# Performance work log

Hardware: AMD Instinct MI355X
Metric: run time of the kernel (lower is better)

The kernel has to match this reference:

```python
import jax, jax.numpy as jnp
import numpy as np

B, C, H, W = 2, 256, 32, 32
PK, CK = 256, 256


def setup_inputs() -> dict:
    key = jax.random.key(0)
    ks = jax.random.split(key, 9)
    s = 1.0 / np.sqrt(C)
    return {
        'x': jax.random.normal(ks[0], (B, C, H, W), jnp.float32),
        'primary_indices': jax.random.randint(ks[1], (B, PK), 0, B * H * W),
        'compare_indices': jax.random.randint(ks[2], (B, CK), 0, B * H * W),
        'pre_w': jax.random.uniform(ks[3], (3, C, C), jnp.float32, -s, s),
        'pre_b': jax.random.uniform(ks[4], (3, C), jnp.float32, -s, s),
        'post_w': jax.random.uniform(ks[5], (2, C, C), jnp.float32, -s, s),
        'post_b': jax.random.uniform(ks[6], (2, C), jnp.float32, -s, s),
        'post_out_w': jax.random.uniform(ks[7], (2, C), jnp.float32, -s, s),
        'post_out_b': jax.random.uniform(ks[8], (2,), jnp.float32, -s, s),
    }


def reference(x, primary_indices, compare_indices, pre_w, pre_b,
              post_w, post_b, post_out_w, post_out_b):
    # pre_compare: stack of 1x1 convs (c->c->c->c), ReLU between layers
    h = x
    for i in range(3):
        h = jnp.einsum('bchw,oc->bohw', h, pre_w[i]) + pre_b[i][None, :, None, None]
        if i < 2:
            h = jax.nn.relu(h)
    bs, c, hh, ww = h.shape
    # flatten to [bs*h*w, c] node features (matches torch transpose+reshape)
    flat = h.reshape(bs, c, hh * ww).transpose(0, 2, 1).reshape(bs * hh * ww, c)
    # gather primary / compare node features with global flat indices
    xp = flat[primary_indices.reshape(-1)].reshape(bs, -1, c).transpose(0, 2, 1)  # [b,c,pk]
    xc = flat[compare_indices.reshape(-1)].reshape(bs, -1, c).transpose(0, 2, 1)  # [b,c,ck]
    # broadcast pairwise squared difference -> [b,c,pk,ck]
    xx = (xp[:, :, :, None] - xc[:, :, None, :]) ** 2
    # post_compare: 1x1 conv stack c->c->c->2, ReLU between layers
    g = xx
    for i in range(2):
        g = jax.nn.relu(jnp.einsum('bcpq,oc->bopq', g, post_w[i]) + post_b[i][None, :, None, None])
    out = jnp.einsum('bcpq,oc->bopq', g, post_out_w) + post_out_b[None, :, None, None]
    return out  # [b, 2, pk, ck]
```

## Files before the change

kernel.cpp:

```cpp
#include <hip/hip_runtime.h>

typedef unsigned short u16;
typedef short bf16x8 __attribute__((ext_vector_type(8)));
typedef float f32x4 __attribute__((ext_vector_type(4)));
typedef u16 u16x4 __attribute__((ext_vector_type(4)));

__device__ __forceinline__ float b2f(u16 h) {
  unsigned u = ((unsigned)h) << 16;
  return __builtin_bit_cast(float, u);
}
__device__ __forceinline__ u16 f2b(float f) {
  return __builtin_bit_cast(u16, (__bf16)f);
}
__device__ __forceinline__ void gld_lds16(const void* g, void* l) {
  __builtin_amdgcn_global_load_lds(
      (__attribute__((address_space(1))) void*)(g),
      (__attribute__((address_space(3))) void*)(l), 16, 0, 0);
}

__global__ void dense_edge_prep(const float* __restrict__ x,
                                const float* __restrict__ pre_w,
                                const float* __restrict__ post_w,
                                u16* __restrict__ wb, u16* __restrict__ xt) {
  const int blk = blockIdx.x;
  const int t = threadIdx.x;
  if (blk < 160) {
    const int id = blk * 256 + t;
    const int layer = id >> 13;
    const int sid = id & 8191;
    const int m = sid >> 5;
    const int s8 = sid & 31;
    const float* src = (layer < 2) ? (post_w + layer * 65536)
                                   : (pre_w + (layer - 2) * 65536);
    u16* dst = wb + layer * 65536;
    f32x4 a = *(const f32x4*)(src + m * 256 + s8 * 8);
    f32x4 c = *(const f32x4*)(src + m * 256 + s8 * 8 + 4);
    bf16x8 o;
#pragma unroll
    for (int j = 0; j < 4; j++) o[j] = (short)f2b(a[j]);
#pragma unroll
    for (int j = 0; j < 4; j++) o[4 + j] = (short)f2b(c[j]);
    *(bf16x8*)(dst + (s8 * 256 + m) * 8) = o;
  } else {
    __shared__ float tile[32 * 65];
    const int xb = blk - 160;
    const int b = xb >> 7;
    const int ct = (xb >> 4) & 7;
    const int ht = xb & 15;
    const int c0 = ct * 32, hw0 = ht * 64;
#pragma unroll
    for (int rep = 0; rep < 8; rep++) {
      const int idx = rep * 256 + t;
      const int cl = idx >> 6, hl = idx & 63;
      tile[cl * 65 + hl] = x[(b * 256 + c0 + cl) * 1024 + hw0 + hl];
    }
    __syncthreads();
    const int hl = t >> 2, c8 = t & 3;
    bf16x8 o;
#pragma unroll
    for (int i = 0; i < 8; i++) o[i] = (short)f2b(tile[(c8 * 8 + i) * 65 + hl]);
    *(bf16x8*)(xt + (b * 1024 + hw0 + hl) * 256 + c0 + c8 * 8) = o;
  }
}

__global__ __launch_bounds__(256, 2) void dense_edge_pre(
    const u16* __restrict__ xt, const u16* __restrict__ wpre,
    const float* __restrict__ preb, u16* __restrict__ flat) {
  __shared__ u16 feat[2][4096];
  const int t = threadIdx.x;
  const int wv = t >> 6, ln = t & 63;
  const int nb = blockIdx.x * 16;
  const int q4 = ln >> 4, r15 = ln & 15;

#pragma unroll
  for (int i = 0; i < 2; i++) {
    const int slot = wv * 128 + i * 64 + ln;
    const int s8 = slot >> 4, nl = slot & 15;
    gld_lds16(xt + (nb + nl) * 256 + s8 * 8, &feat[0][slot * 8]);
  }
  __syncthreads();

#pragma unroll
  for (int l = 0; l < 3; l++) {
    const u16* wl = wpre + l * 65536;
    f32x4 acc[4];
    f32x4 zero = {0.f, 0.f, 0.f, 0.f};
#pragma unroll
    for (int mt = 0; mt < 4; mt++) acc[mt] = zero;
#pragma unroll
    for (int s = 0; s < 8; s++) {
      bf16x8 bv = *(const bf16x8*)(&feat[l & 1][((s * 4 + q4) * 16 + r15) * 8]);
#pragma unroll
      for (int mt = 0; mt < 4; mt++) {
        bf16x8 av = *(const bf16x8*)(wl + ((s * 4 + q4) * 256 + wv * 64 + mt * 16 + r15) * 8);
        acc[mt] = __builtin_amdgcn_mfma_f32_16x16x32_bf16(av, bv, acc[mt], 0, 0, 0);
      }
    }
    if (l < 2) {
#pragma unroll
      for (int mt = 0; mt < 4; mt++) {
        const int o = wv * 64 + mt * 16 + q4 * 4;
        f32x4 bb = *(const f32x4*)(preb + l * 256 + o);
        u16x4 pk;
#pragma unroll
        for (int r = 0; r < 4; r++) {
          float v = fmaxf(acc[mt][r] + bb[r], 0.f);
          pk[r] = f2b(v);
        }
        *(u16x4*)(&feat[(l + 1) & 1][((o >> 3) * 16 + r15) * 8 + (o & 7)]) = pk;
      }
      __syncthreads();
    } else {
#pragma unroll
      for (int mt = 0; mt < 4; mt++) {
        const int o = wv * 64 + mt * 16 + q4 * 4;
        f32x4 bb = *(const f32x4*)(preb + 512 + o);
        u16x4 pk;
#pragma unroll
        for (int r = 0; r < 4; r++) pk[r] = f2b(acc[mt][r] + bb[r]);
        *(u16x4*)(flat + (nb + r15) * 256 + o) = pk;
      }
    }
  }
}

#define NT 8
__global__ __launch_bounds__(1024, 4) void dense_edge_main(
    const u16* __restrict__ flat, const int* __restrict__ pidx,
    const int* __restrict__ cidx, const u16* __restrict__ w1s,
    const u16* __restrict__ w2s, const float* __restrict__ b1,
    const float* __restrict__ b2, const float* __restrict__ w3,
    const float* __restrict__ b3, float* __restrict__ out) {
  __shared__ u16 xxbuf[16384];
  __shared__ u16 t1buf[16384];
  __shared__ u16 pstage[2048];
  __shared__ u16 qstage[2][2048];
  __shared__ float pbuf[8][2][64];

  const int t = threadIdx.x;
  const int wv = t >> 6;
  const int ln = t & 63;
  const int q4 = ln >> 4, r15 = ln & 15;
  const bool prod = wv < 8;
  const int w8 = wv & 7;
  const int blk = blockIdx.x;
  const int tile0 = blk * NT;
  const int b = tile0 >> 10;
  const int pt = (tile0 >> 5) & 31;
  const int qt0 = tile0 & 31;
  const int p0 = pt * 8;

  const u16* wsrc = prod ? w1s : w2s;
  bf16x8 af_w[2][8];
#pragma unroll
  for (int s = 0; s < 8; s++)
#pragma unroll
    for (int mt = 0; mt < 2; mt++)
      af_w[mt][s] = *(const bf16x8*)(wsrc + ((s * 4 + q4) * 256 + w8 * 32 + mt * 16 + r15) * 8);

  if (prod) {
    const int slot = (w8 & 3) * 64 + ln;
    const int row = slot & 7, cc = slot >> 3;
    if (w8 < 4) {
      const int pn = pidx[b * 256 + p0 + row];
      gld_lds16(flat + pn * 256 + cc * 8, &pstage[slot * 8]);
    } else {
      const int qn = cidx[b * 256 + qt0 * 8 + row];
      gld_lds16(flat + qn * 256 + cc * 8, &qstage[0][slot * 8]);
    }
  }
  __syncthreads();

#pragma unroll 1
  for (int j = 0; j <= NT; j++) {
    if (prod) {
      if (j < NT) {
        const bool restage = (j < NT - 1) && (w8 >= 4);
        int qn_next = 0, rslot = 0;
        if (restage) {
          rslot = (w8 - 4) * 64 + ln;
          qn_next = cidx[b * 256 + (qt0 + j + 1) * 8 + (rslot & 7)];
        }
        const u16* qs = qstage[j & 1];
        const int prow = ln >> 3, qrow = ln & 7;
#pragma unroll
        for (int i = 0; i < 4; i++) {
          const int cc = w8 * 4 + i;
          bf16x8 av = *(const bf16x8*)(&pstage[(cc * 8 + prow) * 8]);
          bf16x8 bv = *(const bf16x8*)(&qs[(cc * 8 + qrow) * 8]);
          bf16x8 ov;
#pragma unroll
          for (int jj = 0; jj < 8; jj++) {
            float d = b2f((u16)av[jj]) - b2f((u16)bv[jj]);
            ov[jj] = (short)f2b(d * d);
          }
          *(bf16x8*)(xxbuf + ((cc)*64 + ln) * 8) = ov;
        }
        if (restage)
          gld_lds16(flat + qn_next * 256 + (rslot >> 3) * 8,
                    &qstage[(j + 1) & 1][rslot * 8]);
      }
    } else if (j > 0) {
      f32x4 acc[2][4];
      {
        f32x4 zero = {0.f, 0.f, 0.f, 0.f};
#pragma unroll
        for (int mt = 0; mt < 2; mt++)
#pragma unroll
          for (int nt = 0; nt < 4; nt++) acc[mt][nt] = zero;
      }
#pragma unroll
      for (int s = 0; s < 8; s++) {
        bf16x8 bfr[4];
#pragma unroll
        for (int nt = 0; nt < 4; nt++)
          bfr[nt] = *(const bf16x8*)(t1buf + ((s * 4 + q4) * 64 + nt * 16 + r15) * 8);
#pragma unroll
        for (int mt = 0; mt < 2; mt++)
#pragma unroll
          for (int nt = 0; nt < 4; nt++)
            acc[mt][nt] = __builtin_amdgcn_mfma_f32_16x16x32_bf16(af_w[mt][s], bfr[nt], acc[mt][nt], 0, 0, 0);
      }
      float part[2][4] = {{0.f, 0.f, 0.f, 0.f}, {0.f, 0.f, 0.f, 0.f}};
#pragma unroll
      for (int mt = 0; mt < 2; mt++) {
        const int o = w8 * 32 + mt * 16 + q4 * 4;
        f32x4 bb = *(const f32x4*)(b2 + o);
        f32x4 w3a = *(const f32x4*)(w3 + o);
        f32x4 w3b = *(const f32x4*)(w3 + 256 + o);
#pragma unroll
        for (int nt = 0; nt < 4; nt++) {
#pragma unroll
          for (int r = 0; r < 4; r++) {
            float v = fmaxf(acc[mt][nt][r] + bb[r], 0.f);
            part[0][nt] += v * w3a[r];
            part[1][nt] += v * w3b[r];
          }
        }
      }
#pragma unroll
      for (int o3 = 0; o3 < 2; o3++)
#pragma unroll
        for (int nt = 0; nt < 4; nt++) {
          part[o3][nt] += __shfl_xor(part[o3][nt], 16, 64);
          part[o3][nt] += __shfl_xor(part[o3][nt], 32, 64);
        }
      if (q4 == 0) {
#pragma unroll
        for (int o3 = 0; o3 < 2; o3++)
#pragma unroll
          for (int nt = 0; nt < 4; nt++)
            pbuf[w8][o3][nt * 16 + r15] = part[o3][nt];
      }
    }
    __syncthreads();

    if (prod) {
      if (j < NT) {
        f32x4 acc[2][4];
        {
          f32x4 zero = {0.f, 0.f, 0.f, 0.f};
#pragma unroll
          for (int mt = 0; mt < 2; mt++)
#pragma unroll
            for (int nt = 0; nt < 4; nt++) acc[mt][nt] = zero;
        }
#pragma unroll
        for (int s = 0; s < 8; s++) {
          bf16x8 bfr[4];
#pragma unroll
          for (int nt = 0; nt < 4; nt++)
            bfr[nt] = *(const bf16x8*)(xxbuf + ((s * 4 + q4) * 64 + nt * 16 + r15) * 8);
#pragma unroll
          for (int mt = 0; mt < 2; mt++)
#pragma unroll
            for (int nt = 0; nt < 4; nt++)
              acc[mt][nt] = __builtin_amdgcn_mfma_f32_16x16x32_bf16(af_w[mt][s], bfr[nt], acc[mt][nt], 0, 0, 0);
        }
#pragma unroll
        for (int mt = 0; mt < 2; mt++) {
          const int o = w8 * 32 + mt * 16 + q4 * 4;
          f32x4 bb = *(const f32x4*)(b1 + o);
#pragma unroll
          for (int nt = 0; nt < 4; nt++) {
            const int nn = nt * 16 + r15;
            u16x4 pk;
#pragma unroll
            for (int r = 0; r < 4; r++) {
              float v = fmaxf(acc[mt][nt][r] + bb[r], 0.f);
              pk[r] = f2b(v);
            }
            *(u16x4*)(t1buf + ((o >> 3) * 64 + nn) * 8 + (o & 7)) = pk;
          }
        }
      }
    } else if (j > 0) {
      if (wv < 10) {
        const int idx = (wv - 8) * 64 + ln;
        const int o3 = idx >> 6;
        const int n = idx & 63;
        float v = b3[o3];
#pragma unroll
        for (int k = 0; k < 8; k++) v += pbuf[k][o3][n];
        out[((b * 2 + o3) * 256 + p0 + (n >> 3)) * 256 + (qt0 + j - 1) * 8 + (n & 7)] = v;
      }
    }
    __syncthreads();
  }
}

extern "C" void kernel_launch(void* const* d_in, const int* in_sizes, int n_in,
                              void* d_out, int out_size, void* d_ws, size_t ws_size,
                              hipStream_t stream) {
  (void)in_sizes; (void)n_in; (void)out_size; (void)ws_size;
  const float* x          = (const float*)d_in[0];
  const int*   pidx       = (const int*)d_in[1];
  const int*   cidx       = (const int*)d_in[2];
  const float* pre_w      = (const float*)d_in[3];
  const float* pre_b      = (const float*)d_in[4];
  const float* post_w     = (const float*)d_in[5];
  const float* post_b     = (const float*)d_in[6];
  const float* post_out_w = (const float*)d_in[7];
  const float* post_out_b = (const float*)d_in[8];
  float* out = (float*)d_out;

  u16* ws   = (u16*)d_ws;
  u16* wb   = ws;
  u16* w1s  = wb;
  u16* w2s  = wb + 65536;
  u16* wpre = wb + 131072;
  u16* xt   = ws + 327680;
  u16* flat = ws + 851968;

  dense_edge_prep<<<416, 256, 0, stream>>>(x, pre_w, post_w, wb, xt);
  dense_edge_pre<<<128, 256, 0, stream>>>(xt, wpre, pre_b, flat);
  dense_edge_main<<<256, 1024, 0, stream>>>(flat, pidx, cidx, w1s, w2s,
                                            post_b, post_b + 256,
                                            post_out_w, post_out_b, out);
}
```

Baseline: 126.3 us.

## Replace producer/consumer warp split with unified software-pipelined waves

Drops the 16-wave producer/consumer split: each of the 8 waves now holds both weight sets in registers and runs the xx build, layer-1 GEMM and layer-2 GEMM/reduction in one software-pipelined loop. The xx, t1 and partial-sum buffers are double-buffered, so each iteration needs one barrier instead of two, and the final output write is peeled after the loop. Blocks shrink to 512 threads. Keeping both weight fragments raises register pressure per wave, and with fewer waves per block there is less latency hiding.

```diff
diff --git a/kernel.cpp b/kernel.cpp
--- a/kernel.cpp
+++ b/kernel.cpp
@@ -125,24 +125,22 @@
 }
 
 #define NT 8
-__global__ __launch_bounds__(1024, 4) void dense_edge_main(
+__global__ __launch_bounds__(512, 2) void dense_edge_main(
     const u16* __restrict__ flat, const int* __restrict__ pidx,
     const int* __restrict__ cidx, const u16* __restrict__ w1s,
     const u16* __restrict__ w2s, const float* __restrict__ b1,
     const float* __restrict__ b2, const float* __restrict__ w3,
     const float* __restrict__ b3, float* __restrict__ out) {
-  __shared__ u16 xxbuf[16384];
-  __shared__ u16 t1buf[16384];
+  __shared__ u16 xxbuf[2][16384];
+  __shared__ u16 t1buf[2][16384];
   __shared__ u16 pstage[2048];
   __shared__ u16 qstage[2][2048];
-  __shared__ float pbuf[8][2][64];
+  __shared__ float pbuf[2][8][2][64];
 
   const int t = threadIdx.x;
   const int wv = t >> 6;
   const int ln = t & 63;
   const int q4 = ln >> 4, r15 = ln & 15;
-  const bool prod = wv < 8;
-  const int w8 = wv & 7;
   const int blk = blockIdx.x;
   const int tile0 = blk * NT;
   const int b = tile0 >> 10;
@@ -150,18 +148,20 @@
   const int qt0 = tile0 & 31;
   const int p0 = pt * 8;
 
-  const u16* wsrc = prod ? w1s : w2s;
-  bf16x8 af_w[2][8];
+  bf16x8 w1f[2][8], w2f[2][8];
 #pragma unroll
   for (int s = 0; s < 8; s++)
 #pragma unroll
-    for (int mt = 0; mt < 2; mt++)
-      af_w[mt][s] = *(const bf16x8*)(wsrc + ((s * 4 + q4) * 256 + w8 * 32 + mt * 16 + r15) * 8);
-
-  if (prod) {
-    const int slot = (w8 & 3) * 64 + ln;
+    for (int mt = 0; mt < 2; mt++) {
+      const int off = ((s * 4 + q4) * 256 + wv * 32 + mt * 16 + r15) * 8;
+      w1f[mt][s] = *(const bf16x8*)(w1s + off);
+      w2f[mt][s] = *(const bf16x8*)(w2s + off);
+    }
+
+  {
+    const int slot = (wv & 3) * 64 + ln;
     const int row = slot & 7, cc = slot >> 3;
-    if (w8 < 4) {
+    if (wv < 4) {
       const int pn = pidx[b * 256 + p0 + row];
       gld_lds16(flat + pn * 256 + cc * 8, &pstage[slot * 8]);
     } else {
@@ -171,36 +171,57 @@
   }
   __syncthreads();
 
+  const int prow = ln >> 3, qrow = ln & 7;
+
+  {
+    const u16* qs = qstage[0];
+#pragma unroll
+    for (int i = 0; i < 4; i++) {
+      const int cc = wv * 4 + i;
+      bf16x8 av = *(const bf16x8*)(&pstage[(cc * 8 + prow) * 8]);
+      bf16x8 bv = *(const bf16x8*)(&qs[(cc * 8 + qrow) * 8]);
+      bf16x8 ov;
+#pragma unroll
+      for (int jj = 0; jj < 8; jj++) {
+        float d = b2f((u16)av[jj]) - b2f((u16)bv[jj]);
+        ov[jj] = (short)f2b(d * d);
+      }
+      *(bf16x8*)(&xxbuf[0][(cc * 64 + ln) * 8]) = ov;
+    }
+    if (wv >= 4) {
+      const int slot = (wv - 4) * 64 + ln;
+      const int qn = cidx[b * 256 + (qt0 + 1) * 8 + (slot & 7)];
+      gld_lds16(flat + qn * 256 + (slot >> 3) * 8, &qstage[1][slot * 8]);
+    }
+  }
+  __syncthreads();
+
 #pragma unroll 1
   for (int j = 0; j <= NT; j++) {
-    if (prod) {
-      if (j < NT) {
-        const bool restage = (j < NT - 1) && (w8 >= 4);
-        int qn_next = 0, rslot = 0;
-        if (restage) {
-          rslot = (w8 - 4) * 64 + ln;
-          qn_next = cidx[b * 256 + (qt0 + j + 1) * 8 + (rslot & 7)];
-        }
-        const u16* qs = qstage[j & 1];
-        const int prow = ln >> 3, qrow = ln & 7;
-#pragma unroll
-        for (int i = 0; i < 4; i++) {
-          const int cc = w8 * 4 + i;
-          bf16x8 av = *(const bf16x8*)(&pstage[(cc * 8 + prow) * 8]);
-          bf16x8 bv = *(const bf16x8*)(&qs[(cc * 8 + qrow) * 8]);
-          bf16x8 ov;
-#pragma unroll
-          for (int jj = 0; jj < 8; jj++) {
-            float d = b2f((u16)av[jj]) - b2f((u16)bv[jj]);
-            ov[jj] = (short)f2b(d * d);
-          }
-          *(bf16x8*)(xxbuf + ((cc)*64 + ln) * 8) = ov;
-        }
-        if (restage)
-          gld_lds16(flat + qn_next * 256 + (rslot >> 3) * 8,
-                    &qstage[(j + 1) & 1][rslot * 8]);
-      }
-    } else if (j > 0) {
+    if (j < NT - 1) {
+      const u16* qs = qstage[(j + 1) & 1];
+#pragma unroll
+      for (int i = 0; i < 4; i++) {
+        const int cc = wv * 4 + i;
+        bf16x8 av = *(const bf16x8*)(&pstage[(cc * 8 + prow) * 8]);
+        bf16x8 bv = *(const bf16x8*)(&qs[(cc * 8 + qrow) * 8]);
+        bf16x8 ov;
+#pragma unroll
+        for (int jj = 0; jj < 8; jj++) {
+          float d = b2f((u16)av[jj]) - b2f((u16)bv[jj]);
+          ov[jj] = (short)f2b(d * d);
+        }
+        *(bf16x8*)(&xxbuf[(j + 1) & 1][(cc * 64 + ln) * 8]) = ov;
+      }
+    }
+    if (j < NT - 2 && wv >= 4) {
+      const int slot = (wv - 4) * 64 + ln;
+      const int qn = cidx[b * 256 + (qt0 + j + 2) * 8 + (slot & 7)];
+      gld_lds16(flat + qn * 256 + (slot >> 3) * 8,
+                &qstage[(j + 2) & 1][slot * 8]);
+    }
+    if (j < NT) {
+      const u16* xb = xxbuf[j & 1];
       f32x4 acc[2][4];
       {
         f32x4 zero = {0.f, 0.f, 0.f, 0.f};
@@ -214,17 +235,57 @@
         bf16x8 bfr[4];
 #pragma unroll
         for (int nt = 0; nt < 4; nt++)
-          bfr[nt] = *(const bf16x8*)(t1buf + ((s * 4 + q4) * 64 + nt * 16 + r15) * 8);
+          bfr[nt] = *(const bf16x8*)(xb + ((s * 4 + q4) * 64 + nt * 16 + r15) * 8);
 #pragma unroll
         for (int mt = 0; mt < 2; mt++)
 #pragma unroll
           for (int nt = 0; nt < 4; nt++)
-            acc[mt][nt] = __builtin_amdgcn_mfma_f32_16x16x32_bf16(af_w[mt][s], bfr[nt], acc[mt][nt], 0, 0, 0);
+            acc[mt][nt] = __builtin_amdgcn_mfma_f32_16x16x32_bf16(w1f[mt][s], bfr[nt], acc[mt][nt], 0, 0, 0);
+      }
+#pragma unroll
+      for (int mt = 0; mt < 2; mt++) {
+        const int o = wv * 32 + mt * 16 + q4 * 4;
+        f32x4 bb = *(const f32x4*)(b1 + o);
+#pragma unroll
+        for (int nt = 0; nt < 4; nt++) {
+          const int nn = nt * 16 + r15;
+          u16x4 pk;
+#pragma unroll
+          for (int r = 0; r < 4; r++) {
+            float v = fmaxf(acc[mt][nt][r] + bb[r], 0.f);
+            pk[r] = f2b(v);
+          }
+          *(u16x4*)(&t1buf[j & 1][((o >> 3) * 64 + nn) * 8 + (o & 7)]) = pk;
+        }
+      }
+    }
+    if (j > 0) {
+      const int jm = j - 1;
+      const u16* tb = t1buf[jm & 1];
+      f32x4 acc[2][4];
+      {
+        f32x4 zero = {0.f, 0.f, 0.f, 0.f};
+#pragma unroll
+        for (int mt = 0; mt < 2; mt++)
+#pragma unroll
+          for (int nt = 0; nt < 4; nt++) acc[mt][nt] = zero;
+      }
+#pragma unroll
+      for (int s = 0; s < 8; s++) {
+        bf16x8 bfr[4];
+#pragma unroll
+        for (int nt = 0; nt < 4; nt++)
+          bfr[nt] = *(const bf16x8*)(tb + ((s * 4 + q4) * 64 + nt * 16 + r15) * 8);
+#pragma unroll
+        for (int mt = 0; mt < 2; mt++)
+#pragma unroll
+          for (int nt = 0; nt < 4; nt++)
+            acc[mt][nt] = __builtin_amdgcn_mfma_f32_16x16x32_bf16(w2f[mt][s], bfr[nt], acc[mt][nt], 0, 0, 0);
       }
       float part[2][4] = {{0.f, 0.f, 0.f, 0.f}, {0.f, 0.f, 0.f, 0.f}};
 #pragma unroll
       for (int mt = 0; mt < 2; mt++) {
-        const int o = w8 * 32 + mt * 16 + q4 * 4;
+        const int o = wv * 32 + mt * 16 + q4 * 4;
         f32x4 bb = *(const f32x4*)(b2 + o);
         f32x4 w3a = *(const f32x4*)(w3 + o);
         f32x4 w3b = *(const f32x4*)(w3 + 256 + o);
@@ -250,62 +311,29 @@
         for (int o3 = 0; o3 < 2; o3++)
 #pragma unroll
           for (int nt = 0; nt < 4; nt++)
-            pbuf[w8][o3][nt * 16 + r15] = part[o3][nt];
-      }
+            pbuf[jm & 1][wv][o3][nt * 16 + r15] = part[o3][nt];
+      }
+    }
+    if (j >= 2 && t < 128) {
+      const int jo = j - 2;
+      const int o3 = t >> 6;
+      const int n = t & 63;
+      float v = b3[o3];
+#pragma unroll
+      for (int k = 0; k < 8; k++) v += pbuf[jo & 1][k][o3][n];
+      out[((b * 2 + o3) * 256 + p0 + (n >> 3)) * 256 + (qt0 + jo) * 8 + (n & 7)] = v;
     }
     __syncthreads();
-
-    if (prod) {
-      if (j < NT) {
-        f32x4 acc[2][4];
-        {
-          f32x4 zero = {0.f, 0.f, 0.f, 0.f};
-#pragma unroll
-          for (int mt = 0; mt < 2; mt++)
-#pragma unroll
-            for (int nt = 0; nt < 4; nt++) acc[mt][nt] = zero;
-        }
-#pragma unroll
-        for (int s = 0; s < 8; s++) {
-          bf16x8 bfr[4];
-#pragma unroll
-          for (int nt = 0; nt < 4; nt++)
-            bfr[nt] = *(const bf16x8*)(xxbuf + ((s * 4 + q4) * 64 + nt * 16 + r15) * 8);
-#pragma unroll
-          for (int mt = 0; mt < 2; mt++)
-#pragma unroll
-            for (int nt = 0; nt < 4; nt++)
-              acc[mt][nt] = __builtin_amdgcn_mfma_f32_16x16x32_bf16(af_w[mt][s], bfr[nt], acc[mt][nt], 0, 0, 0);
-        }
-#pragma unroll
-        for (int mt = 0; mt < 2; mt++) {
-          const int o = w8 * 32 + mt * 16 + q4 * 4;
-          f32x4 bb = *(const f32x4*)(b1 + o);
-#pragma unroll
-          for (int nt = 0; nt < 4; nt++) {
-            const int nn = nt * 16 + r15;
-            u16x4 pk;
-#pragma unroll
-            for (int r = 0; r < 4; r++) {
-              float v = fmaxf(acc[mt][nt][r] + bb[r], 0.f);
-              pk[r] = f2b(v);
-            }
-            *(u16x4*)(t1buf + ((o >> 3) * 64 + nn) * 8 + (o & 7)) = pk;
-          }
-        }
-      }
-    } else if (j > 0) {
-      if (wv < 10) {
-        const int idx = (wv - 8) * 64 + ln;
-        const int o3 = idx >> 6;
-        const int n = idx & 63;
-        float v = b3[o3];
-#pragma unroll
-        for (int k = 0; k < 8; k++) v += pbuf[k][o3][n];
-        out[((b * 2 + o3) * 256 + p0 + (n >> 3)) * 256 + (qt0 + j - 1) * 8 + (n & 7)] = v;
-      }
-    }
-    __syncthreads();
+  }
+
+  if (t < 128) {
+    const int jo = NT - 1;
+    const int o3 = t >> 6;
+    const int n = t & 63;
+    float v = b3[o3];
+#pragma unroll
+    for (int k = 0; k < 8; k++) v += pbuf[jo & 1][k][o3][n];
+    out[((b * 2 + o3) * 256 + p0 + (n >> 3)) * 256 + (qt0 + jo) * 8 + (n & 7)] = v;
   }
 }
 
@@ -334,7 +362,7 @@
 
   dense_edge_prep<<<416, 256, 0, stream>>>(x, pre_w, post_w, wb, xt);
   dense_edge_pre<<<128, 256, 0, stream>>>(xt, wpre, pre_b, flat);
-  dense_edge_main<<<256, 1024, 0, stream>>>(flat, pidx, cidx, w1s, w2s,
-                                            post_b, post_b + 256,
-                                            post_out_w, post_out_b, out);
-}
+  dense_edge_main<<<256, 512, 0, stream>>>(flat, pidx, cidx, w1s, w2s,
+                                           post_b, post_b + 256,
+                                           post_out_w, post_out_b, out);
+}
```

Result: faster. 119.5 us (-5.4%).
